# Performance work log

Measured on AMD Instinct MI355X. Metric: run time of the kernel, lower is better.

## Reference

```python
import jax, jax.numpy as jnp
import numpy as np

D_MODEL, H, D_K, D_V, D_FF = 1024, 16, 64, 64, 4096
B, L = 2, 2048
EPS = 1e-5


def layer_norm(x, g, b):
    mu = jnp.mean(x, axis=-1, keepdims=True)
    var = jnp.mean(jnp.square(x - mu), axis=-1, keepdims=True)
    return (x - mu) * jax.lax.rsqrt(var + EPS) * g + b


def setup_inputs() -> dict:
    key = jax.random.key(0)
    ks = jax.random.split(key, 12)
    s = 0.02
    x = jax.random.normal(ks[0], (B, L, D_MODEL), dtype=jnp.float32)
    Wq = jax.random.normal(ks[1], (H, D_MODEL, D_K), dtype=jnp.float32) * s
    Wk = jax.random.normal(ks[2], (H, D_MODEL, D_K), dtype=jnp.float32) * s
    Wv = jax.random.normal(ks[3], (H, D_MODEL, D_V), dtype=jnp.float32) * s
    bq = jnp.zeros((H, D_K), dtype=jnp.float32)
    bk = jnp.zeros((H, D_K), dtype=jnp.float32)
    bv = jnp.zeros((H, D_V), dtype=jnp.float32)
    Wo = jax.random.normal(ks[4], (H * D_V, D_MODEL), dtype=jnp.float32) * s
    W1 = jax.random.normal(ks[5], (D_MODEL, D_FF), dtype=jnp.float32) * s
    b1 = jnp.zeros((D_FF,), dtype=jnp.float32)
    W2 = jax.random.normal(ks[6], (D_FF, D_MODEL), dtype=jnp.float32) * s
    ln1_g = jnp.ones((D_MODEL,), dtype=jnp.float32)
    ln1_b = jnp.zeros((D_MODEL,), dtype=jnp.float32)
    ln2_g = jnp.ones((D_MODEL,), dtype=jnp.float32)
    ln2_b = jnp.zeros((D_MODEL,), dtype=jnp.float32)
    return dict(x=x, Wq=Wq, bq=bq, Wk=Wk, bk=bk, Wv=Wv, bv=bv, Wo=Wo,
                ln1_g=ln1_g, ln1_b=ln1_b, W1=W1, b1=b1, W2=W2,
                ln2_g=ln2_g, ln2_b=ln2_b)


def reference(x, Wq, bq, Wk, bk, Wv, bv, Wo, ln1_g, ln1_b, W1, b1, W2, ln2_g, ln2_b):
    # Batched multi-head attention (all heads at once, equivalent to the
    # per-head Python loop in the original module).
    Q = jnp.einsum('bld,hdk->bhlk', x, Wq) + bq[None, :, None, :]
    K = jnp.einsum('bld,hdk->bhlk', x, Wk) + bk[None, :, None, :]
    V = jnp.einsum('bld,hdv->bhlv', x, Wv) + bv[None, :, None, :]
    scores = jnp.einsum('bhlk,bhmk->bhlm', Q, K) * (1.0 / jnp.sqrt(jnp.float32(D_K)))
    attn = jax.nn.softmax(scores, axis=-1)
    O = jnp.einsum('bhlm,bhmv->bhlv', attn, V)        # [b,h,l,dv]
    O = jnp.transpose(O, (0, 2, 1, 3)).reshape(x.shape[0], x.shape[1], H * D_V)
    mha = O @ Wo                                       # [b,l,d_model]
    # residual + LayerNorm (dropout_prob=0 -> identity)
    h1 = layer_norm(x + mha, ln1_g, ln1_b)
    ff = jax.nn.relu(h1 @ W1 + b1) @ W2
    return layer_norm(h1 + ff, ln2_g, ln2_b)
```

## Files before the change

### kernel.cpp

```cpp
#include <hip/hip_runtime.h>

typedef unsigned short u16;
typedef unsigned int u32;
typedef short bf16x8 __attribute__((ext_vector_type(8)));
typedef float f32x4 __attribute__((ext_vector_type(4)));
typedef unsigned int u32x2 __attribute__((ext_vector_type(2)));

#define D_MODEL 1024
#define NH 16
#define DK 64
#define DFF 4096
#define BATCH 2
#define SEQ 2048
#define BL (BATCH*SEQ)
#define NQKV 3072
#define Q_SCALE 0.18033688011f

__device__ __forceinline__ float bfraw2f(u16 u) {
    union { u32 i; float f; } c; c.i = ((u32)u) << 16; return c.f;
}
__device__ __forceinline__ u16 f2bfraw(float f) {
    union { float f; u32 i; } c; c.f = f;
    u32 i = c.i;
    u32 lsb = (i >> 16) & 1u;
    i += 0x7fffu + lsb;
    return (u16)(i >> 16);
}
__device__ __forceinline__ u32 fasu(float f) {
    union { float f; u32 i; } c; c.f = f; return c.i;
}
__device__ __forceinline__ u32 pack_bf2(float lo, float hi) {
    return __builtin_amdgcn_perm(fasu(hi) + 0x8000u, fasu(lo) + 0x8000u,
                                 0x07060302u);
}
__device__ __forceinline__ void gload_lds16(const u16* g, u16* l) {
    __builtin_amdgcn_global_load_lds(
        (const __attribute__((address_space(1))) void*)g,
        (__attribute__((address_space(3))) void*)l, 16, 0, 0);
}

__global__ __launch_bounds__(256) void cast_f32_bf16(const float* __restrict__ in,
                                                     u16* __restrict__ out) {
    int i = (blockIdx.x * 256 + threadIdx.x) * 4;
    f32x4 v = *(const f32x4*)&in[i];
#pragma unroll
    for (int j = 0; j < 4; j++) out[i + j] = f2bfraw(v[j]);
}


__global__ __launch_bounds__(256) void transpose2d(const float* __restrict__ in,
                                                   u16* __restrict__ out,
                                                   int R, int C) {
    __shared__ u16 t[64][65];
    int c0 = blockIdx.x * 64, r0 = blockIdx.y * 64;
    int col = threadIdx.x & 63, rr = threadIdx.x >> 6;
    for (int i = rr; i < 64; i += 4)
        t[i][col] = f2bfraw(in[(size_t)(r0 + i) * C + c0 + col]);
    __syncthreads();
    for (int i = rr; i < 64; i += 4)
        out[(size_t)(c0 + i) * R + r0 + col] = t[col][i];
}

__global__ __launch_bounds__(256) void transpose_wqkv(const float* __restrict__ Wq,
                                                      const float* __restrict__ Wk,
                                                      const float* __restrict__ Wv,
                                                      u16* __restrict__ out) {
    __shared__ u16 t[64][65];
    int d0 = blockIdx.x * 64;
    int h = blockIdx.y;
    int ms = blockIdx.z;
    const float* W = (ms == 0) ? Wq : (ms == 1) ? Wk : Wv;
    const float* src = W + (size_t)h * D_MODEL * DK;
    int col = threadIdx.x & 63, rr = threadIdx.x >> 6;
    for (int i = rr; i < 64; i += 4)
        t[i][col] = f2bfraw(src[(size_t)(d0 + i) * DK + col]);
    __syncthreads();
    u16* dst = out + (size_t)(ms * 1024 + h * 64) * D_MODEL;
    for (int i = rr; i < 64; i += 4)
        dst[(size_t)i * D_MODEL + d0 + col] = t[col][i];
}

__global__ __launch_bounds__(256) void concat_bias(const float* __restrict__ bq,
                                                   const float* __restrict__ bk,
                                                   const float* __restrict__ bv,
                                                   float* __restrict__ out) {
    int i = blockIdx.x * 256 + threadIdx.x;
    out[i] = (i < 1024) ? bq[i] : (i < 2048) ? bk[i - 1024] : bv[i - 2048];
}


template <int OUT_F32, int RELU, int HASBIAS, int SPLITK, int SCALEQ, int VSTORE>
__global__ __launch_bounds__(256, 4) void gemm_bt(const u16* __restrict__ A,
                                                  const u16* __restrict__ Bt,
                                                  const float* __restrict__ bias,
                                                  void* __restrict__ Cout,
                                                  u16* __restrict__ vtout,
                                                  int M, int N, int K) {
    __shared__ __attribute__((aligned(16))) u16 As[128 * 64];
    __shared__ __attribute__((aligned(16))) u16 Bs[128 * 64];
    const int tid = threadIdx.x;
    const int lane = tid & 63, wid = tid >> 6;
    const int quad = lane >> 4, l16 = lane & 15;
    const int m0 = blockIdx.x * 128, n0 = blockIdx.y * 128;
    const int z = (SPLITK > 1) ? blockIdx.z : 0;
    const int Klen = K / SPLITK;
    const int kend = (z + 1) * Klen;
    const int wm = (wid >> 1) * 64, wn = (wid & 1) * 64;

    f32x4 acc[4][4];
#pragma unroll
    for (int i = 0; i < 4; i++)
#pragma unroll
        for (int j = 0; j < 4; j++) acc[i][j] = (f32x4){0.f, 0.f, 0.f, 0.f};

    const int srow = lane >> 3, scol = (lane & 7) * 8;

    for (int kb = z * Klen; kb < kend; kb += 64) {
#pragma unroll
        for (int p = 0; p < 4; p++) {
            int c = wid * 4 + p;
            int row = c * 8 + srow;
            gload_lds16(&A[(size_t)(m0 + row) * K + kb + scol], &As[c * 512]);
            gload_lds16(&Bt[(size_t)(n0 + row) * K + kb + scol], &Bs[c * 512]);
        }
        __syncthreads();
#pragma unroll
        for (int kh = 0; kh < 2; kh++) {
            bf16x8 af[4], bf[4];
#pragma unroll
            for (int t = 0; t < 4; t++) {
                af[t] = *(const bf16x8*)&As[(wm + t * 16 + l16) * 64 + kh * 32 + quad * 8];
                bf[t] = *(const bf16x8*)&Bs[(wn + t * 16 + l16) * 64 + kh * 32 + quad * 8];
            }
#pragma unroll
            for (int i = 0; i < 4; i++)
#pragma unroll
                for (int j = 0; j < 4; j++)
                    acc[i][j] = __builtin_amdgcn_mfma_f32_16x16x32_bf16(
                        af[i], bf[j], acc[i][j], 0, 0, 0);
        }
        __syncthreads();
    }

    if (VSTORE && n0 >= 2048) {
#pragma unroll
        for (int i = 0; i < 4; i++) {
            int row0 = m0 + wm + i * 16 + quad * 4;
            int bb = row0 >> 11, l = row0 & 2047;
#pragma unroll
            for (int j = 0; j < 4; j++) {
                int col = n0 + wn + j * 16 + l16;
                float bv = HASBIAS ? bias[col] : 0.f;
                int dv = col - 2048;
                u32x2 w;
                w.x = pack_bf2(acc[i][j][0] + bv, acc[i][j][1] + bv);
                w.y = pack_bf2(acc[i][j][2] + bv, acc[i][j][3] + bv);
                *(u32x2*)&vtout[((size_t)(bb * 1024 + dv)) * 2048 + l] = w;
            }
        }
        return;
    }

    float* outf = (float*)Cout + (size_t)z * M * N;
#pragma unroll
    for (int i = 0; i < 4; i++) {
#pragma unroll
        for (int j = 0; j < 4; j++) {
#pragma unroll
            for (int r = 0; r < 4; r++) {
                int row = m0 + wm + i * 16 + quad * 4 + r;
                int col = n0 + wn + j * 16 + l16;
                float v = acc[i][j][r];
                if (HASBIAS) v += bias[col];
                if (RELU) v = v > 0.f ? v : 0.f;
                if (SCALEQ && col < 1024) v *= Q_SCALE;
                if (OUT_F32)
                    outf[(size_t)row * N + col] = v;
                else
                    ((u16*)Cout)[(size_t)row * N + col] = f2bfraw(v);
            }
        }
    }
}

__global__ __launch_bounds__(256, 2) void attn_kernel(const u16* __restrict__ qkv,
                                                      const u16* __restrict__ vt,
                                                      u16* __restrict__ O) {
    __shared__ __attribute__((aligned(16))) u16 Ks[128 * 64];
    __shared__ __attribute__((aligned(16))) u16 Vs[64 * 128];
    __shared__ __attribute__((aligned(16))) u16 Ps[4][32 * 128];

    const int tid = threadIdx.x;
    const int lane = tid & 63, wid = tid >> 6;
    const int quad = lane >> 4, l16 = lane & 15;
    const int sw = l16 & 7;
    const int b = blockIdx.z, h = blockIdx.y;
    const int q0 = blockIdx.x * 128 + wid * 32;

    bf16x8 qf[2][2];
#pragma unroll
    for (int qt = 0; qt < 2; qt++) {
        const size_t qrow = (size_t)(b * SEQ + q0 + qt * 16 + l16) * NQKV + h * DK;
        qf[qt][0] = *(const bf16x8*)&qkv[qrow + quad * 8];
        qf[qt][1] = *(const bf16x8*)&qkv[qrow + 32 + quad * 8];
    }
    const u16* Kbase = qkv + (size_t)(b * SEQ) * NQKV + D_MODEL + h * DK;
    const u16* Vbase = vt + (size_t)((b * NH + h) * DK) * SEQ;

    f32x4 oacc[4][2];
#pragma unroll
    for (int d = 0; d < 4; d++) {
        oacc[d][0] = (f32x4){0.f, 0.f, 0.f, 0.f};
        oacc[d][1] = (f32x4){0.f, 0.f, 0.f, 0.f};
    }
    float lr[2] = {0.f, 0.f};
    const f32x4 Z = {0.f, 0.f, 0.f, 0.f};

    bf16x8 kreg[4], vreg[4];
    auto stage_load = [&](int kt2) {
#pragma unroll
        for (int p = 0; p < 4; p++) {
            int s = p * 256 + tid;
            kreg[p] = *(const bf16x8*)&Kbase[(size_t)(kt2 + (s >> 3)) * NQKV + (s & 7) * 8];
            vreg[p] = *(const bf16x8*)&Vbase[(size_t)(s >> 4) * SEQ + kt2 + (s & 15) * 8];
        }
    };
    stage_load(0);

    for (int kt = 0; kt < SEQ; kt += 128) {
#pragma unroll
        for (int p = 0; p < 4; p++) {
            int s = p * 256 + tid;
            int kr = s >> 3, kc = s & 7;
            *(bf16x8*)&Ks[kr * 64 + ((kc ^ (kr & 7)) * 8)] = kreg[p];
            int vr = s >> 4, vc = s & 15;
            *(bf16x8*)&Vs[vr * 128 + ((vc ^ (vr & 7)) * 8)] = vreg[p];
        }
        __syncthreads();

        if (kt + 128 < SEQ) stage_load(kt + 128);

        f32x4 sacc[8][2];
        __builtin_amdgcn_s_setprio(1);
#pragma unroll
        for (int nt = 0; nt < 8; nt++) {
            const u16* krow = &Ks[(nt * 16 + l16) * 64];
            bf16x8 kf0 = *(const bf16x8*)&krow[(quad ^ sw) * 8];
            bf16x8 kf1 = *(const bf16x8*)&krow[((4 + quad) ^ sw) * 8];
#pragma unroll
            for (int qt = 0; qt < 2; qt++) {
                f32x4 s0 = __builtin_amdgcn_mfma_f32_16x16x32_bf16(kf0, qf[qt][0], Z, 0, 0, 0);
                sacc[nt][qt] = __builtin_amdgcn_mfma_f32_16x16x32_bf16(kf1, qf[qt][1], s0, 0, 0, 0);
            }
        }
        __builtin_amdgcn_s_setprio(0);

#pragma unroll
        for (int qt = 0; qt < 2; qt++) {
            u16* prow = &Ps[wid][(qt * 16 + l16) * 128];
#pragma unroll
            for (int nt = 0; nt < 8; nt++) {
                float p0 = __builtin_amdgcn_exp2f(sacc[nt][qt][0]);
                float p1 = __builtin_amdgcn_exp2f(sacc[nt][qt][1]);
                float p2 = __builtin_amdgcn_exp2f(sacc[nt][qt][2]);
                float p3 = __builtin_amdgcn_exp2f(sacc[nt][qt][3]);
                lr[qt] += (p0 + p1) + (p2 + p3);
                u32x2 w;
                w.x = pack_bf2(p0, p1);
                w.y = pack_bf2(p2, p3);
                int c = nt * 2 + (quad >> 1);
                *(u32x2*)&prow[((c ^ sw) * 8) + (quad & 1) * 4] = w;
            }
        }

        __builtin_amdgcn_s_setprio(1);
#pragma unroll
        for (int ks = 0; ks < 4; ks++) {
            int c = ks * 4 + quad;
            bf16x8 pf0 = *(const bf16x8*)&Ps[wid][l16 * 128 + ((c ^ sw) * 8)];
            bf16x8 pf1 = *(const bf16x8*)&Ps[wid][(16 + l16) * 128 + ((c ^ sw) * 8)];
#pragma unroll
            for (int d = 0; d < 4; d++) {
                bf16x8 vf = *(const bf16x8*)&Vs[(d * 16 + l16) * 128 + ((c ^ sw) * 8)];
                oacc[d][0] = __builtin_amdgcn_mfma_f32_16x16x32_bf16(vf, pf0, oacc[d][0], 0, 0, 0);
                oacc[d][1] = __builtin_amdgcn_mfma_f32_16x16x32_bf16(vf, pf1, oacc[d][1], 0, 0, 0);
            }
        }
        __builtin_amdgcn_s_setprio(0);
        __syncthreads();
    }

#pragma unroll
    for (int qt = 0; qt < 2; qt++) {
        lr[qt] += __shfl_xor(lr[qt], 16, 64);
        lr[qt] += __shfl_xor(lr[qt], 32, 64);
    }

#pragma unroll
    for (int qt = 0; qt < 2; qt++) {
        float iv = 1.f / lr[qt];
        size_t row = (size_t)(b * SEQ + q0 + qt * 16 + l16);
#pragma unroll
        for (int d = 0; d < 4; d++) {
            float o0 = oacc[d][qt][0] * iv, o1 = oacc[d][qt][1] * iv;
            float o2 = oacc[d][qt][2] * iv, o3 = oacc[d][qt][3] * iv;
            u32x2 w;
            w.x = ((u32)f2bfraw(o1) << 16) | f2bfraw(o0);
            w.y = ((u32)f2bfraw(o3) << 16) | f2bfraw(o2);
            *(u32x2*)&O[row * D_MODEL + h * DK + d * 16 + quad * 4] = w;
        }
    }
}

__global__ __launch_bounds__(256) void ln3_kernel(const float* __restrict__ xa,
                                                  const float* __restrict__ xb,
                                                  const float* __restrict__ xc,
                                                  const float* __restrict__ g,
                                                  const float* __restrict__ be,
                                                  u16* __restrict__ out_bf,
                                                  float* __restrict__ out_f) {
    int row = blockIdx.x;
    int tid = threadIdx.x;
    const float* pa = xa + (size_t)row * D_MODEL;
    const float* pb = xb + (size_t)row * D_MODEL;
    const float* pc = xc + (size_t)row * D_MODEL;
    int c = tid * 4;
    f32x4 av = *(const f32x4*)&pa[c];
    f32x4 bv = *(const f32x4*)&pb[c];
    f32x4 cv = *(const f32x4*)&pc[c];
    float v[4];
    float s = 0.f, ss = 0.f;
#pragma unroll
    for (int i = 0; i < 4; i++) {
        v[i] = av[i] + bv[i] + cv[i];
        s += v[i];
        ss += v[i] * v[i];
    }
#pragma unroll
    for (int off = 32; off; off >>= 1) {
        s += __shfl_down(s, off, 64);
        ss += __shfl_down(ss, off, 64);
    }
    __shared__ float red[8];
    int wid = tid >> 6, lane = tid & 63;
    if (lane == 0) { red[wid] = s; red[4 + wid] = ss; }
    __syncthreads();
    if (tid == 0) {
        red[0] = red[0] + red[1] + red[2] + red[3];
        red[4] = red[4] + red[5] + red[6] + red[7];
    }
    __syncthreads();
    float mu = red[0] * (1.f / D_MODEL);
    float var = red[4] * (1.f / D_MODEL) - mu * mu;
    float rs = rsqrtf(var + 1e-5f);
#pragma unroll
    for (int i = 0; i < 4; i++) {
        float o = (v[i] - mu) * rs * g[c + i] + be[c + i];
        if (out_f) out_f[(size_t)row * D_MODEL + c + i] = o;
        if (out_bf) out_bf[(size_t)row * D_MODEL + c + i] = f2bfraw(o);
    }
}

extern "C" void kernel_launch(void* const* d_in, const int* in_sizes, int n_in,
                              void* d_out, int out_size, void* d_ws, size_t ws_size,
                              hipStream_t stream) {
    const float* x   = (const float*)d_in[0];
    const float* Wq  = (const float*)d_in[1];
    const float* bq  = (const float*)d_in[2];
    const float* Wk  = (const float*)d_in[3];
    const float* bk  = (const float*)d_in[4];
    const float* Wv  = (const float*)d_in[5];
    const float* bv  = (const float*)d_in[6];
    const float* Wo  = (const float*)d_in[7];
    const float* g1  = (const float*)d_in[8];
    const float* be1 = (const float*)d_in[9];
    const float* W1  = (const float*)d_in[10];
    const float* b1  = (const float*)d_in[11];
    const float* W2  = (const float*)d_in[12];
    const float* g2  = (const float*)d_in[13];
    const float* be2 = (const float*)d_in[14];

    char* w = (char*)d_ws;
    auto alloc = [&](size_t bytes) {
        char* p = w;
        w += (bytes + 255) & ~(size_t)255;
        return p;
    };
    u16* wqkv_t = (u16*)alloc((size_t)NQKV * D_MODEL * 2);
    u16* wo_t   = (u16*)alloc((size_t)D_MODEL * D_MODEL * 2);
    u16* w1_t   = (u16*)alloc((size_t)DFF * D_MODEL * 2);
    u16* w2_t   = (u16*)alloc((size_t)D_MODEL * DFF * 2);
    float* bqkv = (float*)alloc((size_t)NQKV * 4);
    u16* x_bf   = (u16*)alloc((size_t)BL * D_MODEL * 2);
    u16* qkvbuf = (u16*)alloc((size_t)BL * NQKV * 2);
    u16* vtbuf  = (u16*)alloc((size_t)BATCH * NH * DK * SEQ * 2);
    u16* obuf   = (u16*)alloc((size_t)BL * D_MODEL * 2);
    float* mha_p = (float*)alloc((size_t)2 * BL * D_MODEL * 4);
    u16* h1_bf  = (u16*)alloc((size_t)BL * D_MODEL * 2);
    float* h1_f = (float*)alloc((size_t)BL * D_MODEL * 4);
    u16* ffa    = (u16*)alloc((size_t)BL * DFF * 2);
    float* ffb_p = (float*)alloc((size_t)2 * BL * D_MODEL * 4);

    cast_f32_bf16<<<dim3(BL * D_MODEL / 1024), 256, 0, stream>>>(x, x_bf);
    transpose_wqkv<<<dim3(16, 16, 3), 256, 0, stream>>>(Wq, Wk, Wv, wqkv_t);
    transpose2d<<<dim3(16, 16), 256, 0, stream>>>(Wo, wo_t, 1024, 1024);
    transpose2d<<<dim3(64, 16), 256, 0, stream>>>(W1, w1_t, 1024, 4096);
    transpose2d<<<dim3(16, 64), 256, 0, stream>>>(W2, w2_t, 4096, 1024);
    concat_bias<<<dim3(12), 256, 0, stream>>>(bq, bk, bv, bqkv);

    gemm_bt<0, 0, 1, 1, 1, 1><<<dim3(32, 24), 256, 0, stream>>>(
        x_bf, wqkv_t, bqkv, qkvbuf, vtbuf, BL, NQKV, D_MODEL);
    attn_kernel<<<dim3(16, 16, 2), 256, 0, stream>>>(qkvbuf, vtbuf, obuf);
    gemm_bt<1, 0, 0, 2, 0, 0><<<dim3(32, 8, 2), 256, 0, stream>>>(
        obuf, wo_t, nullptr, mha_p, nullptr, BL, D_MODEL, D_MODEL);
    ln3_kernel<<<dim3(BL), 256, 0, stream>>>(x, mha_p, mha_p + (size_t)BL * D_MODEL,
                                             g1, be1, h1_bf, h1_f);
    gemm_bt<0, 1, 1, 1, 0, 0><<<dim3(32, 32), 256, 0, stream>>>(
        h1_bf, w1_t, b1, ffa, nullptr, BL, DFF, D_MODEL);
    gemm_bt<1, 0, 0, 2, 0, 0><<<dim3(32, 8, 2), 256, 0, stream>>>(
        ffa, w2_t, nullptr, ffb_p, nullptr, BL, D_MODEL, DFF);
    ln3_kernel<<<dim3(BL), 256, 0, stream>>>(h1_f, ffb_p, ffb_p + (size_t)BL * D_MODEL,
                                             g2, be2, nullptr, (float*)d_out);
}
```

Before: 373.4 us.

## Restructure attention: 8 waves of 16 queries, register-resident P, async K loads

```diff
diff --git a/kernel.cpp b/kernel.cpp
--- a/kernel.cpp
+++ b/kernel.cpp
@@ -5,6 +5,7 @@
 typedef short bf16x8 __attribute__((ext_vector_type(8)));
 typedef float f32x4 __attribute__((ext_vector_type(4)));
 typedef unsigned int u32x2 __attribute__((ext_vector_type(2)));
+typedef unsigned int u32x4 __attribute__((ext_vector_type(4)));
 
 #define D_MODEL 1024
 #define NH 16
@@ -183,132 +184,130 @@
     }
 }
 
-__global__ __launch_bounds__(256, 2) void attn_kernel(const u16* __restrict__ qkv,
+__global__ __launch_bounds__(512, 4) void attn_kernel(const u16* __restrict__ qkv,
                                                       const u16* __restrict__ vt,
                                                       u16* __restrict__ O) {
-    __shared__ __attribute__((aligned(16))) u16 Ks[128 * 64];
+    __shared__ __attribute__((aligned(16))) u16 Ks[2][128 * 64];
     __shared__ __attribute__((aligned(16))) u16 Vs[64 * 128];
-    __shared__ __attribute__((aligned(16))) u16 Ps[4][32 * 128];
 
     const int tid = threadIdx.x;
     const int lane = tid & 63, wid = tid >> 6;
     const int quad = lane >> 4, l16 = lane & 15;
     const int sw = l16 & 7;
     const int b = blockIdx.z, h = blockIdx.y;
-    const int q0 = blockIdx.x * 128 + wid * 32;
-
-    bf16x8 qf[2][2];
-#pragma unroll
-    for (int qt = 0; qt < 2; qt++) {
-        const size_t qrow = (size_t)(b * SEQ + q0 + qt * 16 + l16) * NQKV + h * DK;
-        qf[qt][0] = *(const bf16x8*)&qkv[qrow + quad * 8];
-        qf[qt][1] = *(const bf16x8*)&qkv[qrow + 32 + quad * 8];
-    }
+    const int q0 = blockIdx.x * 128 + wid * 16;
+
+    const size_t qrow = (size_t)(b * SEQ + q0 + l16) * NQKV + h * DK;
+    const bf16x8 qf0 = *(const bf16x8*)&qkv[qrow + quad * 8];
+    const bf16x8 qf1 = *(const bf16x8*)&qkv[qrow + 32 + quad * 8];
+
     const u16* Kbase = qkv + (size_t)(b * SEQ) * NQKV + D_MODEL + h * DK;
     const u16* Vbase = vt + (size_t)((b * NH + h) * DK) * SEQ;
 
-    f32x4 oacc[4][2];
-#pragma unroll
-    for (int d = 0; d < 4; d++) {
-        oacc[d][0] = (f32x4){0.f, 0.f, 0.f, 0.f};
-        oacc[d][1] = (f32x4){0.f, 0.f, 0.f, 0.f};
-    }
-    float lr[2] = {0.f, 0.f};
+    f32x4 oacc[4];
+#pragma unroll
+    for (int d = 0; d < 4; d++) oacc[d] = (f32x4){0.f, 0.f, 0.f, 0.f};
+    float lr = 0.f;
     const f32x4 Z = {0.f, 0.f, 0.f, 0.f};
 
-    bf16x8 kreg[4], vreg[4];
-    auto stage_load = [&](int kt2) {
-#pragma unroll
-        for (int p = 0; p < 4; p++) {
-            int s = p * 256 + tid;
-            kreg[p] = *(const bf16x8*)&Kbase[(size_t)(kt2 + (s >> 3)) * NQKV + (s & 7) * 8];
+    auto stage_k = [&](int kt2, int buf) {
+#pragma unroll
+        for (int p = 0; p < 2; p++) {
+            int seg = p * 8 + wid;
+            int row = seg * 8 + (lane >> 3);
+            int chunk = (lane & 7) ^ (lane >> 3);
+            gload_lds16(&Kbase[(size_t)(kt2 + row) * NQKV + chunk * 8],
+                        &Ks[buf][seg * 512]);
+        }
+    };
+    bf16x8 vreg[2];
+    auto load_v = [&](int kt2) {
+#pragma unroll
+        for (int p = 0; p < 2; p++) {
+            int s = p * 512 + tid;
             vreg[p] = *(const bf16x8*)&Vbase[(size_t)(s >> 4) * SEQ + kt2 + (s & 15) * 8];
         }
     };
-    stage_load(0);
-
-    for (int kt = 0; kt < SEQ; kt += 128) {
-#pragma unroll
-        for (int p = 0; p < 4; p++) {
-            int s = p * 256 + tid;
-            int kr = s >> 3, kc = s & 7;
-            *(bf16x8*)&Ks[kr * 64 + ((kc ^ (kr & 7)) * 8)] = kreg[p];
+    stage_k(0, 0);
+    load_v(0);
+
+    for (int t = 0; t < SEQ / 128; t++) {
+        const int kt = t * 128;
+#pragma unroll
+        for (int p = 0; p < 2; p++) {
+            int s = p * 512 + tid;
             int vr = s >> 4, vc = s & 15;
-            *(bf16x8*)&Vs[vr * 128 + ((vc ^ (vr & 7)) * 8)] = vreg[p];
+            int chunkA = (vc >> 2) * 4 + (vc & 1) * 2;
+            int rem = ((vc >> 1) & 1) * 4;
+            u32x4 kv = __builtin_bit_cast(u32x4, vreg[p]);
+            *(u32x2*)&Vs[vr * 128 + ((chunkA ^ (vr & 7)) * 8) + rem] =
+                (u32x2){kv.x, kv.y};
+            *(u32x2*)&Vs[vr * 128 + (((chunkA + 1) ^ (vr & 7)) * 8) + rem] =
+                (u32x2){kv.z, kv.w};
         }
         __syncthreads();
 
-        if (kt + 128 < SEQ) stage_load(kt + 128);
-
-        f32x4 sacc[8][2];
+        if (t + 1 < SEQ / 128) {
+            stage_k(kt + 128, (t + 1) & 1);
+            load_v(kt + 128);
+        }
+
+        const u16* kb = Ks[t & 1];
+
+        f32x4 sacc[8];
         __builtin_amdgcn_s_setprio(1);
 #pragma unroll
         for (int nt = 0; nt < 8; nt++) {
-            const u16* krow = &Ks[(nt * 16 + l16) * 64];
+            const u16* krow = &kb[(nt * 16 + l16) * 64];
             bf16x8 kf0 = *(const bf16x8*)&krow[(quad ^ sw) * 8];
             bf16x8 kf1 = *(const bf16x8*)&krow[((4 + quad) ^ sw) * 8];
-#pragma unroll
-            for (int qt = 0; qt < 2; qt++) {
-                f32x4 s0 = __builtin_amdgcn_mfma_f32_16x16x32_bf16(kf0, qf[qt][0], Z, 0, 0, 0);
-                sacc[nt][qt] = __builtin_amdgcn_mfma_f32_16x16x32_bf16(kf1, qf[qt][1], s0, 0, 0, 0);
-            }
+            f32x4 s0 = __builtin_amdgcn_mfma_f32_16x16x32_bf16(kf0, qf0, Z, 0, 0, 0);
+            sacc[nt] = __builtin_amdgcn_mfma_f32_16x16x32_bf16(kf1, qf1, s0, 0, 0, 0);
         }
         __builtin_amdgcn_s_setprio(0);
 
-#pragma unroll
-        for (int qt = 0; qt < 2; qt++) {
-            u16* prow = &Ps[wid][(qt * 16 + l16) * 128];
-#pragma unroll
-            for (int nt = 0; nt < 8; nt++) {
-                float p0 = __builtin_amdgcn_exp2f(sacc[nt][qt][0]);
-                float p1 = __builtin_amdgcn_exp2f(sacc[nt][qt][1]);
-                float p2 = __builtin_amdgcn_exp2f(sacc[nt][qt][2]);
-                float p3 = __builtin_amdgcn_exp2f(sacc[nt][qt][3]);
-                lr[qt] += (p0 + p1) + (p2 + p3);
-                u32x2 w;
-                w.x = pack_bf2(p0, p1);
-                w.y = pack_bf2(p2, p3);
-                int c = nt * 2 + (quad >> 1);
-                *(u32x2*)&prow[((c ^ sw) * 8) + (quad & 1) * 4] = w;
-            }
+        u32 wreg[8][2];
+#pragma unroll
+        for (int nt = 0; nt < 8; nt++) {
+            float p0 = __builtin_amdgcn_exp2f(sacc[nt][0]);
+            float p1 = __builtin_amdgcn_exp2f(sacc[nt][1]);
+            float p2 = __builtin_amdgcn_exp2f(sacc[nt][2]);
+            float p3 = __builtin_amdgcn_exp2f(sacc[nt][3]);
+            lr += (p0 + p1) + (p2 + p3);
+            wreg[nt][0] = pack_bf2(p0, p1);
+            wreg[nt][1] = pack_bf2(p2, p3);
         }
 
         __builtin_amdgcn_s_setprio(1);
 #pragma unroll
         for (int ks = 0; ks < 4; ks++) {
-            int c = ks * 4 + quad;
-            bf16x8 pf0 = *(const bf16x8*)&Ps[wid][l16 * 128 + ((c ^ sw) * 8)];
-            bf16x8 pf1 = *(const bf16x8*)&Ps[wid][(16 + l16) * 128 + ((c ^ sw) * 8)];
+            u32x4 pw = (u32x4){wreg[2 * ks][0], wreg[2 * ks][1],
+                               wreg[2 * ks + 1][0], wreg[2 * ks + 1][1]};
+            bf16x8 pf = __builtin_bit_cast(bf16x8, pw);
 #pragma unroll
             for (int d = 0; d < 4; d++) {
-                bf16x8 vf = *(const bf16x8*)&Vs[(d * 16 + l16) * 128 + ((c ^ sw) * 8)];
-                oacc[d][0] = __builtin_amdgcn_mfma_f32_16x16x32_bf16(vf, pf0, oacc[d][0], 0, 0, 0);
-                oacc[d][1] = __builtin_amdgcn_mfma_f32_16x16x32_bf16(vf, pf1, oacc[d][1], 0, 0, 0);
+                bf16x8 vf = *(const bf16x8*)&Vs[(d * 16 + l16) * 128 +
+                                                (((ks * 4 + quad) ^ sw) * 8)];
+                oacc[d] = __builtin_amdgcn_mfma_f32_16x16x32_bf16(vf, pf, oacc[d], 0, 0, 0);
             }
         }
         __builtin_amdgcn_s_setprio(0);
         __syncthreads();
     }
 
-#pragma unroll
-    for (int qt = 0; qt < 2; qt++) {
-        lr[qt] += __shfl_xor(lr[qt], 16, 64);
-        lr[qt] += __shfl_xor(lr[qt], 32, 64);
-    }
-
-#pragma unroll
-    for (int qt = 0; qt < 2; qt++) {
-        float iv = 1.f / lr[qt];
-        size_t row = (size_t)(b * SEQ + q0 + qt * 16 + l16);
-#pragma unroll
-        for (int d = 0; d < 4; d++) {
-            float o0 = oacc[d][qt][0] * iv, o1 = oacc[d][qt][1] * iv;
-            float o2 = oacc[d][qt][2] * iv, o3 = oacc[d][qt][3] * iv;
-            u32x2 w;
-            w.x = ((u32)f2bfraw(o1) << 16) | f2bfraw(o0);
-            w.y = ((u32)f2bfraw(o3) << 16) | f2bfraw(o2);
-            *(u32x2*)&O[row * D_MODEL + h * DK + d * 16 + quad * 4] = w;
-        }
+    lr += __shfl_xor(lr, 16, 64);
+    lr += __shfl_xor(lr, 32, 64);
+    float iv = 1.f / lr;
+
+    size_t row = (size_t)(b * SEQ + q0 + l16);
+#pragma unroll
+    for (int d = 0; d < 4; d++) {
+        float o0 = oacc[d][0] * iv, o1 = oacc[d][1] * iv;
+        float o2 = oacc[d][2] * iv, o3 = oacc[d][3] * iv;
+        u32x2 w;
+        w.x = ((u32)f2bfraw(o1) << 16) | f2bfraw(o0);
+        w.y = ((u32)f2bfraw(o3) << 16) | f2bfraw(o2);
+        *(u32x2*)&O[row * D_MODEL + h * DK + d * 16 + quad * 4] = w;
     }
 }
 
@@ -410,7 +409,7 @@
 
     gemm_bt<0, 0, 1, 1, 1, 1><<<dim3(32, 24), 256, 0, stream>>>(
         x_bf, wqkv_t, bqkv, qkvbuf, vtbuf, BL, NQKV, D_MODEL);
-    attn_kernel<<<dim3(16, 16, 2), 256, 0, stream>>>(qkvbuf, vtbuf, obuf);
+    attn_kernel<<<dim3(16, 16, 2), 512, 0, stream>>>(qkvbuf, vtbuf, obuf);
     gemm_bt<1, 0, 0, 2, 0, 0><<<dim3(32, 8, 2), 256, 0, stream>>>(
         obuf, wo_t, nullptr, mha_p, nullptr, BL, D_MODEL, D_MODEL);
     ln3_kernel<<<dim3(BL), 256, 0, stream>>>(x, mha_p, mha_p + (size_t)BL * D_MODEL,
```

After: 369.7 us. About the same (-1.0%).
